# Kernel optimization log

Hardware: AMD Instinct MI355X
Metric: run time of the kernel (lower is better)

## Reference

```python
import jax, jax.numpy as jnp
import numpy as np

B, S, D, H = 2, 2048, 1024, 16
DH = D // H              # 64
BLK = S // 16            # 128, default block_size = seq_len // 16
NB = S // BLK            # 16 blocks per axis


def setup_inputs() -> dict:
    key = jax.random.key(0)
    ks = jax.random.split(key, 7)
    scale = 0.02
    x = jax.random.normal(ks[0], (B, S, D), jnp.float32)
    Wq = jax.random.normal(ks[1], (D, D), jnp.float32) * scale
    Wk = jax.random.normal(ks[2], (D, D), jnp.float32) * scale
    Wv = jax.random.normal(ks[3], (D, D), jnp.float32) * scale
    Wo = jax.random.normal(ks[4], (D, D), jnp.float32) * scale
    bo = jnp.zeros((D,), jnp.float32)
    # keep-block decisions: torch.rand(1) > sparsity(=0.5) per (i,j) block
    block_mask = jax.random.randint(ks[5], (NB, NB), 0, 2).astype(bool)
    # keep diagonal blocks so no query row is fully masked (avoids NaN softmax)
    block_mask = block_mask | jnp.eye(NB, dtype=bool)
    return {"x": x, "Wq": Wq, "Wk": Wk, "Wv": Wv, "Wo": Wo, "bo": bo,
            "block_mask": block_mask}


def reference(x, Wq, Wk, Wv, Wo, bo, block_mask):
    # projections (torch Linear: y = x @ W.T), split heads -> [B,H,S,DH]
    def split(t):
        return t.reshape(B, S, H, DH).transpose(0, 2, 1, 3)
    q = split(x @ Wq.T)
    k = split(x @ Wk.T)
    v = split(x @ Wv.T)

    scores = jnp.einsum('bhqd,bhkd->bhqk', q, k) / jnp.sqrt(jnp.float32(DH))
    # expand [NB,NB] block mask to [S,S]; shared across batch and heads
    mask_full = jnp.repeat(jnp.repeat(block_mask, BLK, axis=0), BLK, axis=1)
    scores = jnp.where(mask_full, scores, -jnp.inf)
    attn = jax.nn.softmax(scores, axis=-1)        # dropout = identity (eval)
    out = jnp.einsum('bhqk,bhkd->bhqd', attn, v)
    out = out.transpose(0, 2, 1, 3).reshape(B, S, D)
    return out @ Wo.T + bo
```

## Files before the change

### kernel.cpp

```cpp
#include <hip/hip_runtime.h>
#include <hip/hip_bf16.h>


typedef __attribute__((ext_vector_type(4))) float f32x4;
typedef __attribute__((ext_vector_type(8))) short bf16x8;

#define MFMA16(a, b, c) __builtin_amdgcn_mfma_f32_16x16x32_bf16(a, b, c, 0, 0, 0)
#define LOG2E 1.4426950408889634f

__device__ inline unsigned short f2bf(float f) {
  unsigned u = __builtin_bit_cast(unsigned, f);
  unsigned rounding = 0x7FFFu + ((u >> 16) & 1u);
  return (unsigned short)((u + rounding) >> 16);
}

__global__ __launch_bounds__(256) void cvt_kernel(const float* __restrict__ in,
                                                  unsigned short* __restrict__ out, int n8) {
  const int i = blockIdx.x * 256 + threadIdx.x;
  if (i >= n8) return;
  const float4* p = (const float4*)in + (size_t)i * 2;
  const float4 a = p[0], b = p[1];
  union { unsigned short u[8]; uint4 v; } r;
  r.u[0] = f2bf(a.x); r.u[1] = f2bf(a.y); r.u[2] = f2bf(a.z); r.u[3] = f2bf(a.w);
  r.u[4] = f2bf(b.x); r.u[5] = f2bf(b.y); r.u[6] = f2bf(b.z); r.u[7] = f2bf(b.w);
  *((uint4*)out + i) = r.v;
}

__device__ inline int mask_mode(const void* maskp) {
  const unsigned short* mh = (const unsigned short*)maskp;
  const unsigned* mw = (const unsigned*)maskp;
  bool anyFloatHalf = false;
  for (int t = 0; t < 128; ++t) {
    const unsigned short v = mh[t];
    if (v == 0x3F80u || v == 0x3C00u) { anyFloatHalf = true; break; }
  }
  if (anyFloatHalf) {
    bool evenNZ = false;
    for (int t = 0; t < 128; t += 2)
      if (mh[t] != 0) { evenNZ = true; break; }
    return evenNZ ? 1 : 0;
  }
  bool anyBig = false;
  for (int t = 0; t < 64; ++t)
    if (mw[t] > 1u) { anyBig = true; break; }
  if (anyBig) return 2;
  bool oddNZ = false;
  for (int t = 1; t < 64; t += 2)
    if (mw[t] != 0u) { oddNZ = true; break; }
  return oddNZ ? 3 : 4;
}

__device__ inline int mask_read(const void* maskp, int mode, int idx) {
  switch (mode) {
    case 0: return ((const unsigned*)maskp)[idx] != 0u;
    case 1: return ((const unsigned short*)maskp)[idx] != 0;
    case 2: return ((const unsigned char*)maskp)[idx] != 0;
    case 3: return ((const int*)maskp)[idx] != 0;
    default: return ((const unsigned*)maskp)[idx * 2] != 0u ||
                    ((const unsigned*)maskp)[idx * 2 + 1] != 0u;
  }
}

__device__ inline void stage_tile_128x32(const __hip_bfloat16* g, int ld_elems,
                                         __hip_bfloat16* lds, int wave, int lane) {
#pragma unroll
  for (int i = 0; i < 2; ++i) {
    const int chunk = wave * 2 + i;
    const int o = chunk * 1024 + lane * 16;
    const int r = o >> 6;
    const int cb = o & 63;
    const char* ga = (const char*)g + (size_t)r * ld_elems * 2 + cb;
    __builtin_amdgcn_global_load_lds(
        (const __attribute__((address_space(1))) unsigned int*)ga,
        (__attribute__((address_space(3))) unsigned int*)((char*)lds + chunk * 1024),
        16, 0, 0);
  }
}

template <int MODE>
__global__ __launch_bounds__(256) void gemm_bt(
    const __hip_bfloat16* __restrict__ A,
    const __hip_bfloat16* __restrict__ W0, const __hip_bfloat16* __restrict__ W1,
    const float* __restrict__ bias,
    __hip_bfloat16* __restrict__ OutB, float* __restrict__ OutF, int K) {
  __shared__ __hip_bfloat16 sA[128 * 32];
  __shared__ __hip_bfloat16 sB[128 * 32];
  const int tid = threadIdx.x;
  const int wave = tid >> 6, lane = tid & 63;
  const int lr = lane & 15, lg = lane >> 4;
  const int wr = wave >> 1, wc = wave & 1;
  const int m0 = blockIdx.x * 128;

  const __hip_bfloat16* W;
  __hip_bfloat16* OB = nullptr;
  int n0;
  if (MODE == 0) {
    const int sel = blockIdx.y >> 3;
    n0 = (blockIdx.y & 7) * 128;
    W = sel ? W1 : W0;
    OB = OutB + (size_t)sel * 4194304ull;
  } else {
    n0 = blockIdx.y * 128;
    W = W0;
    OB = OutB;
  }

  f32x4 acc[4][4] = {};
  for (int k0 = 0; k0 < K; k0 += 32) {
    stage_tile_128x32(A + (size_t)m0 * K + k0, K, sA, wave, lane);
    stage_tile_128x32(W + (size_t)n0 * K + k0, K, sB, wave, lane);
    __syncthreads();

    bf16x8 af[4], bfr[4];
#pragma unroll
    for (int mi = 0; mi < 4; ++mi)
      af[mi] = *(const bf16x8*)(sA + (64 * wr + 16 * mi + lr) * 32 + lg * 8);
#pragma unroll
    for (int ni = 0; ni < 4; ++ni)
      bfr[ni] = *(const bf16x8*)(sB + (64 * wc + 16 * ni + lr) * 32 + lg * 8);
#pragma unroll
    for (int i = 0; i < 4; ++i)
#pragma unroll
      for (int jj = 0; jj < 4; ++jj)
        acc[i][jj] = (MODE == 2) ? MFMA16(bfr[i], af[jj], acc[i][jj])
                                 : MFMA16(af[i], bfr[jj], acc[i][jj]);
    __syncthreads();
  }

  if (MODE == 2) {
#pragma unroll
    for (int i = 0; i < 4; ++i)
#pragma unroll
      for (int jj = 0; jj < 4; ++jj)
#pragma unroll
        for (int q = 0; q < 4; ++q) {
          const int n = n0 + 64 * wc + 16 * i + lg * 4 + q;
          const int m = m0 + 64 * wr + 16 * jj + lr;
          OB[((size_t)(m >> 11) * 1024 + n) * 2048 + (m & 2047)] =
              __float2bfloat16(acc[i][jj][q]);
        }
  } else {
#pragma unroll
    for (int i = 0; i < 4; ++i)
#pragma unroll
      for (int jj = 0; jj < 4; ++jj)
#pragma unroll
        for (int q = 0; q < 4; ++q) {
          const int m = m0 + 64 * wr + 16 * i + lg * 4 + q;
          const int n = n0 + 64 * wc + 16 * jj + lr;
          if (MODE == 0) OB[(size_t)m * 1024 + n] = __float2bfloat16(acc[i][jj][q]);
          else           OutF[(size_t)m * 1024 + n] = acc[i][jj][q] + bias[n];
        }
  }
}

__global__ __launch_bounds__(256) void attn_kernel(
    const __hip_bfloat16* __restrict__ Q, const __hip_bfloat16* __restrict__ K,
    const __hip_bfloat16* __restrict__ Vt, const void* __restrict__ maskp,
    __hip_bfloat16* __restrict__ O) {
  __shared__ char uKP[4 * 32 * 136 * 2];
  __shared__ char sV[64 * 256];
  __hip_bfloat16 (*P_lds)[32][136] = (__hip_bfloat16(*)[32][136])uKP;

  const int qb = blockIdx.x, bh = blockIdx.y;
  const int b = bh >> 4, h = bh & 15;
  const int tid = threadIdx.x, wave = tid >> 6, lane = tid & 63;
  const int lr = lane & 15, lg = lane >> 4;

  const int mmode = mask_mode(maskp);
  int keep[16], nkeep = 0;
  for (int j = 0; j < 16; ++j)
    if (mask_read(maskp, mmode, qb * 16 + j)) keep[nkeep++] = j;

  const size_t base = (size_t)b * 2048 * 1024 + (size_t)h * 64;
  const char* Kbase  = (const char*)(K + base);
  const char* Vtbase = (const char*)Vt +
      ((size_t)b * 1024 * 2048 + (size_t)h * 64 * 2048) * 2;
  const int qrow0 = qb * 128 + wave * 32;

  bf16x8 qf[2][2];
#pragma unroll
  for (int mt = 0; mt < 2; ++mt)
#pragma unroll
    for (int ks = 0; ks < 2; ++ks)
      qf[mt][ks] = *(const bf16x8*)(Q + base + (size_t)(qrow0 + 16 * mt + lr) * 1024 + ks * 32 + lg * 8);

  f32x4 oa[2][4] = {};
  float mrun[2][4], lrun[2][4];
#pragma unroll
  for (int mt = 0; mt < 2; ++mt)
#pragma unroll
    for (int q = 0; q < 4; ++q) { mrun[mt][q] = -1e30f; lrun[mt][q] = 0.f; }

  for (int ji = 0; ji < nkeep; ++ji) {
    const int j = keep[ji];
    const char* gK = Kbase + (size_t)j * 128 * 2048;
    const char* gV = Vtbase + (size_t)j * 128 * 2;

#pragma unroll
    for (int i = 0; i < 4; ++i) {
      const int o = (wave * 4 + i) * 1024 + lane * 16;
      { const int r = o >> 7, cb = o & 127, cbs = cb ^ ((r & 7) << 4);
        __builtin_amdgcn_global_load_lds(
            (const __attribute__((address_space(1))) unsigned*)(gK + (size_t)r * 2048 + cbs),
            (__attribute__((address_space(3))) unsigned*)(uKP + o), 16, 0, 0); }
      { const int r = o >> 8, cb = o & 255, cbs = cb ^ ((r & 7) << 4);
        __builtin_amdgcn_global_load_lds(
            (const __attribute__((address_space(1))) unsigned*)(gV + (size_t)r * 4096 + cbs),
            (__attribute__((address_space(3))) unsigned*)(sV + o), 16, 0, 0); }
    }
    __syncthreads();

    f32x4 s[2][8] = {};
    __builtin_amdgcn_s_setprio(1);
#pragma unroll
    for (int ks = 0; ks < 2; ++ks)
#pragma unroll
      for (int nt = 0; nt < 8; ++nt) {
        const int row = 16 * nt + lr;
        bf16x8 kf = *(const bf16x8*)(uKP + row * 128 + ((ks * 64 + lg * 16) ^ ((lr & 7) << 4)));
        s[0][nt] = MFMA16(qf[0][ks], kf, s[0][nt]);
        s[1][nt] = MFMA16(qf[1][ks], kf, s[1][nt]);
      }
    __builtin_amdgcn_s_setprio(0);

#pragma unroll
    for (int mt = 0; mt < 2; ++mt) {
#pragma unroll
      for (int q = 0; q < 4; ++q) {
        float rm = -1e30f;
#pragma unroll
        for (int nt = 0; nt < 8; ++nt) {
          s[mt][nt][q] *= 0.125f;
          rm = fmaxf(rm, s[mt][nt][q]);
        }
        rm = fmaxf(rm, __shfl_xor(rm, 1));
        rm = fmaxf(rm, __shfl_xor(rm, 2));
        rm = fmaxf(rm, __shfl_xor(rm, 4));
        rm = fmaxf(rm, __shfl_xor(rm, 8));
        const float mold = mrun[mt][q];
        const float mnew = fmaxf(mold, rm);
        const float sf = exp2f((mold - mnew) * LOG2E);
        float rs = 0.f;
#pragma unroll
        for (int nt = 0; nt < 8; ++nt) {
          const float p = exp2f((s[mt][nt][q] - mnew) * LOG2E);
          s[mt][nt][q] = p;
          rs += p;
        }
        rs += __shfl_xor(rs, 1);
        rs += __shfl_xor(rs, 2);
        rs += __shfl_xor(rs, 4);
        rs += __shfl_xor(rs, 8);
        lrun[mt][q] = lrun[mt][q] * sf + rs;
        mrun[mt][q] = mnew;
#pragma unroll
        for (int ni = 0; ni < 4; ++ni) oa[mt][ni][q] *= sf;
      }
    }

    __syncthreads();

#pragma unroll
    for (int mt = 0; mt < 2; ++mt)
#pragma unroll
      for (int nt = 0; nt < 8; ++nt)
#pragma unroll
        for (int q = 0; q < 4; ++q)
          P_lds[wave][16 * mt + lg * 4 + q][16 * nt + lr] = __float2bfloat16(s[mt][nt][q]);

    __builtin_amdgcn_s_setprio(1);
#pragma unroll
    for (int ks = 0; ks < 4; ++ks) {
      bf16x8 pa0 = *(const bf16x8*)&P_lds[wave][lr][ks * 32 + lg * 8];
      bf16x8 pa1 = *(const bf16x8*)&P_lds[wave][16 + lr][ks * 32 + lg * 8];
#pragma unroll
      for (int ni = 0; ni < 4; ++ni) {
        const int row = 16 * ni + lr;
        bf16x8 vb = *(const bf16x8*)(sV + row * 256 + ((ks * 64 + lg * 16) ^ ((lr & 7) << 4)));
        oa[0][ni] = MFMA16(pa0, vb, oa[0][ni]);
        oa[1][ni] = MFMA16(pa1, vb, oa[1][ni]);
      }
    }
    __builtin_amdgcn_s_setprio(0);
    __syncthreads();
  }

#pragma unroll
  for (int mt = 0; mt < 2; ++mt)
#pragma unroll
    for (int ni = 0; ni < 4; ++ni)
#pragma unroll
      for (int q = 0; q < 4; ++q) {
        const int row = qrow0 + 16 * mt + lg * 4 + q;
        const float v = oa[mt][ni][q] / fmaxf(lrun[mt][q], 1e-30f);
        O[base + (size_t)row * 1024 + 16 * ni + lr] = __float2bfloat16(v);
      }
}

extern "C" void kernel_launch(void* const* d_in, const int* in_sizes, int n_in,
                              void* d_out, int out_size, void* d_ws, size_t ws_size,
                              hipStream_t stream) {
  const float* x  = (const float*)d_in[0];
  const float* Wq = (const float*)d_in[1];
  const float* Wk = (const float*)d_in[2];
  const float* Wv = (const float*)d_in[3];
  const float* Wo = (const float*)d_in[4];
  const float* bo = (const float*)d_in[5];
  const void* mask = d_in[6];
  float* out = (float*)d_out;

  __hip_bfloat16* ws = (__hip_bfloat16*)d_ws;
  __hip_bfloat16* xb  = ws;
  __hip_bfloat16* Wqb = ws + 4194304ull;
  __hip_bfloat16* Wkb = ws + 5242880ull;
  __hip_bfloat16* Wvb = ws + 6291456ull;
  __hip_bfloat16* Wob = ws + 7340032ull;
  __hip_bfloat16* Qb  = ws + 8388608ull;
  __hip_bfloat16* Kb  = ws + 12582912ull;
  __hip_bfloat16* Vtb = ws + 16777216ull;
  __hip_bfloat16* Ob  = ws + 20971520ull;

  dim3 blk(256);
  cvt_kernel<<<2048, blk, 0, stream>>>(x,  (unsigned short*)xb,  524288);
  cvt_kernel<<<512,  blk, 0, stream>>>(Wq, (unsigned short*)Wqb, 131072);
  cvt_kernel<<<512,  blk, 0, stream>>>(Wk, (unsigned short*)Wkb, 131072);
  cvt_kernel<<<512,  blk, 0, stream>>>(Wv, (unsigned short*)Wvb, 131072);
  cvt_kernel<<<512,  blk, 0, stream>>>(Wo, (unsigned short*)Wob, 131072);
  gemm_bt<0><<<dim3(32, 16), blk, 0, stream>>>(xb, Wqb, Wkb, nullptr, Qb, nullptr, 1024);
  gemm_bt<2><<<dim3(32, 8), blk, 0, stream>>>(xb, Wvb, nullptr, nullptr, Vtb, nullptr, 1024);
  attn_kernel<<<dim3(16, 32), blk, 0, stream>>>(Qb, Kb, Vtb, mask, Ob);
  gemm_bt<1><<<dim3(32, 8), blk, 0, stream>>>(Ob, Wob, nullptr, bo, nullptr, out, 1024);
}
```

Measured before the change: 341.2 us.

## Split attention query tiles to 64 rows per block, doubling grid size

The attention kernel now gives each workgroup 64 query rows instead of 128, with each wave handling 16 rows, and the grid doubles to 32x32 blocks. P gets its own LDS buffer instead of aliasing the K tile, which removes one barrier per kept block. This raises parallelism and occupancy (512 to 1024 blocks on the GPU's many CUs) and cuts per-wave register use. In exchange, every K/V tile is loaded from global memory twice as often, and each kf/vb fragment is reused by one MFMA instead of two.

Result: faster. 300.1 us (-12.1%).

```diff
diff --git a/kernel.cpp b/kernel.cpp
--- a/kernel.cpp
+++ b/kernel.cpp
@@ -158,16 +158,17 @@
     const __hip_bfloat16* __restrict__ Q, const __hip_bfloat16* __restrict__ K,
     const __hip_bfloat16* __restrict__ Vt, const void* __restrict__ maskp,
     __hip_bfloat16* __restrict__ O) {
-  __shared__ char uKP[4 * 32 * 136 * 2];
+  __shared__ char uK[128 * 128];
   __shared__ char sV[64 * 256];
-  __hip_bfloat16 (*P_lds)[32][136] = (__hip_bfloat16(*)[32][136])uKP;
-
-  const int qb = blockIdx.x, bh = blockIdx.y;
+  __shared__ __hip_bfloat16 P_lds[4][16][136];
+
+  const int qc = blockIdx.x, bh = blockIdx.y;
   const int b = bh >> 4, h = bh & 15;
   const int tid = threadIdx.x, wave = tid >> 6, lane = tid & 63;
   const int lr = lane & 15, lg = lane >> 4;
 
   const int mmode = mask_mode(maskp);
+  const int qb = qc >> 1;
   int keep[16], nkeep = 0;
   for (int j = 0; j < 16; ++j)
     if (mask_read(maskp, mmode, qb * 16 + j)) keep[nkeep++] = j;
@@ -176,21 +177,17 @@
   const char* Kbase  = (const char*)(K + base);
   const char* Vtbase = (const char*)Vt +
       ((size_t)b * 1024 * 2048 + (size_t)h * 64 * 2048) * 2;
-  const int qrow0 = qb * 128 + wave * 32;
-
-  bf16x8 qf[2][2];
-#pragma unroll
-  for (int mt = 0; mt < 2; ++mt)
-#pragma unroll
-    for (int ks = 0; ks < 2; ++ks)
-      qf[mt][ks] = *(const bf16x8*)(Q + base + (size_t)(qrow0 + 16 * mt + lr) * 1024 + ks * 32 + lg * 8);
-
-  f32x4 oa[2][4] = {};
-  float mrun[2][4], lrun[2][4];
-#pragma unroll
-  for (int mt = 0; mt < 2; ++mt)
-#pragma unroll
-    for (int q = 0; q < 4; ++q) { mrun[mt][q] = -1e30f; lrun[mt][q] = 0.f; }
+  const int qrow0 = qc * 64 + wave * 16;
+
+  bf16x8 qf[2];
+#pragma unroll
+  for (int ks = 0; ks < 2; ++ks)
+    qf[ks] = *(const bf16x8*)(Q + base + (size_t)(qrow0 + lr) * 1024 + ks * 32 + lg * 8);
+
+  f32x4 oa[4] = {};
+  float mrun[4], lrun[4];
+#pragma unroll
+  for (int q = 0; q < 4; ++q) { mrun[q] = -1e30f; lrun[q] = 0.f; }
 
   for (int ji = 0; ji < nkeep; ++ji) {
     const int j = keep[ji];
@@ -203,7 +200,7 @@
       { const int r = o >> 7, cb = o & 127, cbs = cb ^ ((r & 7) << 4);
         __builtin_amdgcn_global_load_lds(
             (const __attribute__((address_space(1))) unsigned*)(gK + (size_t)r * 2048 + cbs),
-            (__attribute__((address_space(3))) unsigned*)(uKP + o), 16, 0, 0); }
+            (__attribute__((address_space(3))) unsigned*)(uK + o), 16, 0, 0); }
       { const int r = o >> 8, cb = o & 255, cbs = cb ^ ((r & 7) << 4);
         __builtin_amdgcn_global_load_lds(
             (const __attribute__((address_space(1))) unsigned*)(gV + (size_t)r * 4096 + cbs),
@@ -211,75 +208,65 @@
     }
     __syncthreads();
 
-    f32x4 s[2][8] = {};
+    f32x4 s[8] = {};
     __builtin_amdgcn_s_setprio(1);
 #pragma unroll
     for (int ks = 0; ks < 2; ++ks)
 #pragma unroll
       for (int nt = 0; nt < 8; ++nt) {
         const int row = 16 * nt + lr;
-        bf16x8 kf = *(const bf16x8*)(uKP + row * 128 + ((ks * 64 + lg * 16) ^ ((lr & 7) << 4)));
-        s[0][nt] = MFMA16(qf[0][ks], kf, s[0][nt]);
-        s[1][nt] = MFMA16(qf[1][ks], kf, s[1][nt]);
+        bf16x8 kf = *(const bf16x8*)(uK + row * 128 + ((ks * 64 + lg * 16) ^ ((lr & 7) << 4)));
+        s[nt] = MFMA16(qf[ks], kf, s[nt]);
       }
     __builtin_amdgcn_s_setprio(0);
 
 #pragma unroll
-    for (int mt = 0; mt < 2; ++mt) {
-#pragma unroll
-      for (int q = 0; q < 4; ++q) {
-        float rm = -1e30f;
-#pragma unroll
-        for (int nt = 0; nt < 8; ++nt) {
-          s[mt][nt][q] *= 0.125f;
-          rm = fmaxf(rm, s[mt][nt][q]);
-        }
-        rm = fmaxf(rm, __shfl_xor(rm, 1));
-        rm = fmaxf(rm, __shfl_xor(rm, 2));
-        rm = fmaxf(rm, __shfl_xor(rm, 4));
-        rm = fmaxf(rm, __shfl_xor(rm, 8));
-        const float mold = mrun[mt][q];
-        const float mnew = fmaxf(mold, rm);
-        const float sf = exp2f((mold - mnew) * LOG2E);
-        float rs = 0.f;
-#pragma unroll
-        for (int nt = 0; nt < 8; ++nt) {
-          const float p = exp2f((s[mt][nt][q] - mnew) * LOG2E);
-          s[mt][nt][q] = p;
-          rs += p;
-        }
-        rs += __shfl_xor(rs, 1);
-        rs += __shfl_xor(rs, 2);
-        rs += __shfl_xor(rs, 4);
-        rs += __shfl_xor(rs, 8);
-        lrun[mt][q] = lrun[mt][q] * sf + rs;
-        mrun[mt][q] = mnew;
-#pragma unroll
-        for (int ni = 0; ni < 4; ++ni) oa[mt][ni][q] *= sf;
+    for (int q = 0; q < 4; ++q) {
+      float rm = -1e30f;
+#pragma unroll
+      for (int nt = 0; nt < 8; ++nt) {
+        s[nt][q] *= 0.125f;
+        rm = fmaxf(rm, s[nt][q]);
       }
+      rm = fmaxf(rm, __shfl_xor(rm, 1));
+      rm = fmaxf(rm, __shfl_xor(rm, 2));
+      rm = fmaxf(rm, __shfl_xor(rm, 4));
+      rm = fmaxf(rm, __shfl_xor(rm, 8));
+      const float mold = mrun[q];
+      const float mnew = fmaxf(mold, rm);
+      const float sf = exp2f((mold - mnew) * LOG2E);
+      float rs = 0.f;
+#pragma unroll
+      for (int nt = 0; nt < 8; ++nt) {
+        const float p = exp2f((s[nt][q] - mnew) * LOG2E);
+        s[nt][q] = p;
+        rs += p;
+      }
+      rs += __shfl_xor(rs, 1);
+      rs += __shfl_xor(rs, 2);
+      rs += __shfl_xor(rs, 4);
+      rs += __shfl_xor(rs, 8);
+      lrun[q] = lrun[q] * sf + rs;
+      mrun[q] = mnew;
+#pragma unroll
+      for (int ni = 0; ni < 4; ++ni) oa[ni][q] *= sf;
     }
 
-    __syncthreads();
-
-#pragma unroll
-    for (int mt = 0; mt < 2; ++mt)
-#pragma unroll
-      for (int nt = 0; nt < 8; ++nt)
-#pragma unroll
-        for (int q = 0; q < 4; ++q)
-          P_lds[wave][16 * mt + lg * 4 + q][16 * nt + lr] = __float2bfloat16(s[mt][nt][q]);
+#pragma unroll
+    for (int nt = 0; nt < 8; ++nt)
+#pragma unroll
+      for (int q = 0; q < 4; ++q)
+        P_lds[wave][lg * 4 + q][16 * nt + lr] = __float2bfloat16(s[nt][q]);
 
     __builtin_amdgcn_s_setprio(1);
 #pragma unroll
     for (int ks = 0; ks < 4; ++ks) {
-      bf16x8 pa0 = *(const bf16x8*)&P_lds[wave][lr][ks * 32 + lg * 8];
-      bf16x8 pa1 = *(const bf16x8*)&P_lds[wave][16 + lr][ks * 32 + lg * 8];
+      bf16x8 pa = *(const bf16x8*)&P_lds[wave][lr][ks * 32 + lg * 8];
 #pragma unroll
       for (int ni = 0; ni < 4; ++ni) {
         const int row = 16 * ni + lr;
         bf16x8 vb = *(const bf16x8*)(sV + row * 256 + ((ks * 64 + lg * 16) ^ ((lr & 7) << 4)));
-        oa[0][ni] = MFMA16(pa0, vb, oa[0][ni]);
-        oa[1][ni] = MFMA16(pa1, vb, oa[1][ni]);
+        oa[ni] = MFMA16(pa, vb, oa[ni]);
       }
     }
     __builtin_amdgcn_s_setprio(0);
@@ -287,15 +274,13 @@
   }
 
 #pragma unroll
-  for (int mt = 0; mt < 2; ++mt)
-#pragma unroll
-    for (int ni = 0; ni < 4; ++ni)
-#pragma unroll
-      for (int q = 0; q < 4; ++q) {
-        const int row = qrow0 + 16 * mt + lg * 4 + q;
-        const float v = oa[mt][ni][q] / fmaxf(lrun[mt][q], 1e-30f);
-        O[base + (size_t)row * 1024 + 16 * ni + lr] = __float2bfloat16(v);
-      }
+  for (int ni = 0; ni < 4; ++ni)
+#pragma unroll
+    for (int q = 0; q < 4; ++q) {
+      const int row = qrow0 + lg * 4 + q;
+      const float v = oa[ni][q] / fmaxf(lrun[q], 1e-30f);
+      O[base + (size_t)row * 1024 + 16 * ni + lr] = __float2bfloat16(v);
+    }
 }
 
 extern "C" void kernel_launch(void* const* d_in, const int* in_sizes, int n_in,
@@ -329,6 +314,6 @@
   cvt_kernel<<<512,  blk, 0, stream>>>(Wo, (unsigned short*)Wob, 131072);
   gemm_bt<0><<<dim3(32, 16), blk, 0, stream>>>(xb, Wqb, Wkb, nullptr, Qb, nullptr, 1024);
   gemm_bt<2><<<dim3(32, 8), blk, 0, stream>>>(xb, Wvb, nullptr, nullptr, Vtb, nullptr, 1024);
-  attn_kernel<<<dim3(16, 32), blk, 0, stream>>>(Qb, Kb, Vtb, mask, Ob);
+  attn_kernel<<<dim3(32, 32), blk, 0, stream>>>(Qb, Kb, Vtb, mask, Ob);
   gemm_bt<1><<<dim3(32, 8), blk, 0, stream>>>(Ob, Wob, nullptr, bo, nullptr, out, 1024);
 }
```
